# Kernel optimization log

Measured on AMD Instinct MI355X. Metric: run time of the kernel, lower is better.

The kernel has to match this reference:

```python
import jax, jax.numpy as jnp
import numpy as np

N = 20000          # num nodes (config['max_nodes'])
R = 11             # num relations = 5*2 + 1
B = 8              # num bases
IN_DIM = 300       # numberbatch embedding size
OUT_DIM = 256      # lstm hidden size
E = 640000         # num edges (avg degree 32)


def setup_inputs() -> dict:
    key = jax.random.key(0)
    k1, k2, k3, k4, k5, k6 = jax.random.split(key, 6)
    features = jax.random.normal(k1, (N, IN_DIM), dtype=jnp.float32)
    comps = jax.random.normal(k2, (R, B), dtype=jnp.float32) * 0.1
    bases = jax.random.normal(k3, (B, IN_DIM, OUT_DIM), dtype=jnp.float32) * 0.05
    bias = jnp.zeros((OUT_DIM,), dtype=jnp.float32)
    edge_src = jax.random.randint(k4, (E,), 0, N, dtype=jnp.int32)
    edge_rel = jax.random.randint(k5, (E,), 0, R, dtype=jnp.int32)
    edge_dst = jax.random.randint(k6, (E,), 0, N, dtype=jnp.int32)
    return {"features": features, "comps": comps, "bases": bases, "bias": bias,
            "edge_src": edge_src, "edge_rel": edge_rel, "edge_dst": edge_dst}


def reference(features, comps, bases, bias, edge_src, edge_rel, edge_dst):
    # Basis decomposition: per-relation weights [R, in, out]
    weights = jnp.einsum('rb,bio->rio', comps, bases)

    # Vertically-stacked sparse adjacency of size [R*N, N]:
    # row = rel*N + src, col = dst, with row normalization (sum_sparse).
    rows = edge_rel * N + edge_src                      # [E]
    ones = jnp.ones((E,), dtype=features.dtype)
    deg = jax.ops.segment_sum(ones, rows, num_segments=R * N)  # row sums
    vals = 1.0 / deg[rows]                              # normalized edge values

    # spmm(adj, features): gather neighbor features, scale, scatter-add to rows
    msgs = features[edge_dst] * vals[:, None]           # [E, in]
    af = jax.ops.segment_sum(msgs, rows, num_segments=R * N)   # [R*N, in]
    af = af.reshape(R, N, IN_DIM)

    # Relation-wise transform and sum over relations
    out = jnp.einsum('rio,rni->no', weights, af) + bias  # [N, out]
    return out
```

## Files before the change

kernel.cpp:

```cpp
#include <hip/hip_runtime.h>

#define NN   20000
#define RR   11
#define BB   8
#define IND  300
#define OUTD 256
#define EE   640000
#define RN   (RR * NN)
#define KP   304
#define SBS  308
#define SBU  (SBS / 2)
#define CAP  32
#define NSCAN_BLOCKS 215
#define SME  768
#define FEATB 5860
#define WT2B  304
#define HZB   860

typedef short bf16x8 __attribute__((ext_vector_type(8)));
typedef float f32x16 __attribute__((ext_vector_type(16)));

union U8 {
    bf16x8  v;
    ushort4 h[2];
    uint4   q;
};

__device__ inline unsigned short f2bf(float f) {
    union { float f; unsigned u; } x;
    x.f = f;
    unsigned u = x.u;
    u += 0x7fffu + ((u >> 16) & 1u);
    return (unsigned short)(u >> 16);
}
__device__ inline float bflo(unsigned p) { return __uint_as_float(p << 16); }
__device__ inline float bfhi(unsigned p) { return __uint_as_float(p & 0xFFFF0000u); }
__device__ inline unsigned packbf(float x, float y) {
    return (unsigned)f2bf(x) | ((unsigned)f2bf(y) << 16);
}

__global__ __launch_bounds__(256) void k_prep(const float* __restrict__ feat,
                                              const float* __restrict__ comps,
                                              const float* __restrict__ bases,
                                              unsigned short* __restrict__ f2,
                                              unsigned short* __restrict__ wt,
                                              unsigned* __restrict__ hist,
                                              int feat_blocks) {
    const int b = blockIdx.x;
    if (b < feat_blocks) {
        const unsigned i = ((unsigned)b * 256u + threadIdx.x) * 4u;
        if (i < (unsigned)(NN * IND)) {
            const float4 v = *(const float4*)(feat + i);
            ushort4 o;
            o.x = f2bf(v.x); o.y = f2bf(v.y); o.z = f2bf(v.z); o.w = f2bf(v.w);
            *(ushort4*)(f2 + i) = o;
        }
        return;
    }
    const int b2 = b - feat_blocks;
    if (b2 < WT2B) {
        const unsigned idx = (unsigned)b2 * 256u + threadIdx.x;
        const unsigned o   = idx / KP;
        const unsigned k   = idx - o * KP;
        float bk[BB];
#pragma unroll
        for (int bb = 0; bb < BB; ++bb)
            bk[bb] = (k < IND) ? bases[((unsigned)bb * IND + k) * OUTD + o] : 0.f;
#pragma unroll
        for (int r = 0; r < RR; ++r) {
            float acc = 0.f;
#pragma unroll
            for (int bb = 0; bb < BB; ++bb) acc += comps[r * BB + bb] * bk[bb];
            wt[((unsigned)r * OUTD + o) * KP + k] = f2bf(acc);
        }
        return;
    }
    const unsigned idx = (unsigned)(b2 - WT2B) * 256u + threadIdx.x;
    if (idx < RN) hist[idx] = 0u;
}

__global__ __launch_bounds__(256) void k_scatter2(const int* __restrict__ esrc,
                                                  const int* __restrict__ erel,
                                                  const int* __restrict__ edst,
                                                  unsigned* __restrict__ cnt,
                                                  unsigned* __restrict__ ssd2) {
    const int e = blockIdx.x * 256 + threadIdx.x;
    const unsigned key = (unsigned)erel[e] * NN + (unsigned)esrc[e];
    const unsigned p = atomicAdd(&cnt[key], 1u);
    if (p < CAP) ssd2[key * CAP + p] = (unsigned)edst[e];
}

__global__ __launch_bounds__(256) void k_hist(const int* __restrict__ esrc,
                                              const int* __restrict__ erel,
                                              unsigned* __restrict__ hist) {
    const int e = blockIdx.x * 256 + threadIdx.x;
    const unsigned key = (unsigned)erel[e] * NN + (unsigned)esrc[e];
    atomicAdd(&hist[key], 1u);
}

__global__ __launch_bounds__(256) void k_scan1(const unsigned* __restrict__ hist,
                                               unsigned* __restrict__ off,
                                               unsigned* __restrict__ bsum) {
    __shared__ unsigned sc[256];
    const int tid = threadIdx.x;
    const unsigned base = blockIdx.x * 1024u + (unsigned)tid * 4u;
    unsigned v0 = (base + 0 < RN) ? hist[base + 0] : 0u;
    unsigned v1 = (base + 1 < RN) ? hist[base + 1] : 0u;
    unsigned v2 = (base + 2 < RN) ? hist[base + 2] : 0u;
    unsigned v3 = (base + 3 < RN) ? hist[base + 3] : 0u;
    const unsigned s = v0 + v1 + v2 + v3;
    sc[tid] = s;
    __syncthreads();
    for (int d = 1; d < 256; d <<= 1) {
        unsigned t = (tid >= d) ? sc[tid - d] : 0u;
        __syncthreads();
        sc[tid] += t;
        __syncthreads();
    }
    if (tid == 255) bsum[blockIdx.x] = sc[255];
    unsigned run = sc[tid] - s;
    if (base + 0 < RN) off[base + 0] = run; run += v0;
    if (base + 1 < RN) off[base + 1] = run; run += v1;
    if (base + 2 < RN) off[base + 2] = run; run += v2;
    if (base + 3 < RN) off[base + 3] = run;
}

__global__ __launch_bounds__(256) void k_scan3(unsigned* __restrict__ off,
                                               unsigned* __restrict__ off2,
                                               const unsigned* __restrict__ bsum) {
    __shared__ unsigned sS;
    const unsigned K = blockIdx.x >> 2;
    if (threadIdx.x < 64) {
        unsigned s = 0;
        for (unsigned i = threadIdx.x; i < K; i += 64u) s += bsum[i];
#pragma unroll
        for (int d = 1; d < 64; d <<= 1) s += __shfl_xor(s, d, 64);
        if (threadIdx.x == 0) sS = s;
    }
    __syncthreads();
    const unsigned idx = blockIdx.x * 256u + threadIdx.x;
    if (idx < RN) {
        const unsigned v = off[idx] + sS;
        off[idx]  = v;
        off2[idx] = v;
    }
    if (idx == 0) off[RN] = EE;
}

__global__ __launch_bounds__(256) void k_scatter(const int* __restrict__ esrc,
                                                 const int* __restrict__ erel,
                                                 const int* __restrict__ edst,
                                                 unsigned* __restrict__ off2,
                                                 unsigned* __restrict__ ssd) {
    const int e = blockIdx.x * 256 + threadIdx.x;
    const unsigned key = (unsigned)erel[e] * NN + (unsigned)esrc[e];
    const unsigned p = atomicAdd(&off2[key], 1u);
    ssd[p] = (unsigned)edst[e];
}

template<int USE_BF16, int FIXED>
__global__ __launch_bounds__(512, 8) void k_main(const float* __restrict__ feat,
                                                 const unsigned short* __restrict__ feat2,
                                                 const float* __restrict__ bias,
                                                 const unsigned* __restrict__ offs,
                                                 const unsigned* __restrict__ ssd,
                                                 const unsigned short* __restrict__ wt,
                                                 float* __restrict__ out) {
    __shared__ __align__(16) unsigned short sbf[32 * SBS];
    __shared__ unsigned sme[FIXED ? 32 * CAP : SME];
    __shared__ unsigned soffs[RR * 33];

    const int tid  = threadIdx.x;
    const int wave = tid >> 6;
    const int lane = tid & 63;
    const int row  = lane & 31;
    const int q    = lane >> 5;
    const int n0   = blockIdx.x * 32;
    const int o0   = wave * 32;

    if (FIXED) {
        if (tid < RR * 32)
            soffs[tid] = offs[(tid >> 5) * NN + n0 + (tid & 31)];
    } else {
        if (tid < RR * 33) {
            const int r = tid / 33, j = tid - r * 33;
            soffs[tid] = offs[r * NN + n0 + j];
        }
    }
    if (tid < 128)
        ((unsigned*)sbf)[(tid >> 2) * SBU + 150 + (tid & 3)] = 0u;

    f32x16 acc;
#pragma unroll
    for (int i = 0; i < 16; ++i) acc[i] = 0.f;

    __syncthreads();

    for (int r = 0; r < RR; ++r) {
        const unsigned* so = soffs + r * (FIXED ? 32 : 33);
        unsigned e0v = 0;
        if (FIXED) {
            const unsigned gbase = ((unsigned)r * NN + (unsigned)n0) * CAP;
            sme[tid]       = ssd[gbase + tid];
            sme[tid + 512] = ssd[gbase + tid + 512];
        } else {
            e0v = so[0];
            const unsigned nE = so[32] - e0v;
            for (unsigned j = (unsigned)tid; j < nE; j += 512u)
                sme[j] = ssd[e0v + j];
        }
        __syncthreads();

#pragma unroll
        for (int g = 0; g < 4; ++g) {
            const int m = wave * 4 + g;
            unsigned c0, c1;
            float inv;
            if (FIXED) {
                const unsigned lenT = so[m];
                c0  = (unsigned)m * CAP;
                c1  = c0 + (lenT < CAP ? lenT : CAP);
                inv = lenT ? 1.0f / (float)lenT : 0.f;
            } else {
                c0  = so[m];
                c1  = so[m + 1];
                inv = (c1 > c0) ? 1.0f / (float)(c1 - c0) : 0.f;
            }
            if (USE_BF16) {
                float a0 = 0, a1 = 0, a2 = 0, a3 = 0, a4 = 0, a5 = 0;
                for (unsigned e = c0; e < c1; ++e) {
                    const unsigned d   = sme[e - e0v];
                    const unsigned* fp = (const unsigned*)feat2 + d * 150u;
                    const unsigned p0 = fp[lane];
                    const unsigned p1 = fp[lane + 64];
                    unsigned p2 = 0u;
                    if (lane < 22) p2 = fp[lane + 128];
                    a0 += bflo(p0); a1 += bfhi(p0);
                    a2 += bflo(p1); a3 += bfhi(p1);
                    a4 += bflo(p2); a5 += bfhi(p2);
                }
                unsigned* sp = (unsigned*)sbf + m * SBU;
                sp[lane]      = packbf(a0 * inv, a1 * inv);
                sp[lane + 64] = packbf(a2 * inv, a3 * inv);
                if (lane < 22) sp[lane + 128] = packbf(a4 * inv, a5 * inv);
            } else {
                float a0 = 0, a1 = 0, a2 = 0, a3 = 0, a4 = 0;
                for (unsigned e = c0; e < c1; ++e) {
                    const unsigned d = sme[e - e0v];
                    const float* fp  = feat + (size_t)d * IND;
                    a0 += fp[lane];
                    a1 += fp[lane + 64];
                    a2 += fp[lane + 128];
                    a3 += fp[lane + 192];
                    if (lane < 44) a4 += fp[lane + 256];
                }
                unsigned short* sp = sbf + m * SBS;
                sp[lane]       = f2bf(a0 * inv);
                sp[lane + 64]  = f2bf(a1 * inv);
                sp[lane + 128] = f2bf(a2 * inv);
                sp[lane + 192] = f2bf(a3 * inv);
                if (lane < 44) sp[lane + 256] = f2bf(a4 * inv);
            }
        }
        __syncthreads();

        const unsigned short* wb = wt + ((size_t)(r * OUTD + o0 + row) * KP) + 8 * q;
        const unsigned short* ab = sbf + row * SBS + 8 * q;
#pragma unroll
        for (int ks = 0; ks < 19; ++ks) {
            const int kk = ks * 16;
            U8 a, b;
            a.h[0] = *(const ushort4*)(ab + kk);
            a.h[1] = *(const ushort4*)(ab + kk + 4);
            b.q    = *(const uint4*)(wb + kk);
            acc = __builtin_amdgcn_mfma_f32_32x32x16_bf16(a.v, b.v, acc, 0, 0, 0);
        }
    }

    const int o = o0 + row;
    const float bv = bias[o];
#pragma unroll
    for (int reg = 0; reg < 16; ++reg) {
        const int node = (reg & 3) + 8 * (reg >> 2) + 4 * q;
        out[(size_t)(n0 + node) * OUTD + o] = acc[reg] + bv;
    }
}

extern "C" void kernel_launch(void* const* d_in, const int* in_sizes, int n_in,
                              void* d_out, int out_size, void* d_ws, size_t ws_size,
                              hipStream_t stream) {
    const float* feat  = (const float*)d_in[0];
    const float* comps = (const float*)d_in[1];
    const float* bases = (const float*)d_in[2];
    const float* bias  = (const float*)d_in[3];
    const int*   esrc  = (const int*)d_in[4];
    const int*   erel  = (const int*)d_in[5];
    const int*   edst  = (const int*)d_in[6];
    float* out = (float*)d_out;

    char* ws = (char*)d_ws;

    if (ws_size >= (size_t)42752192) {
        unsigned short* wt    = (unsigned short*)(ws + 0);
        unsigned*       cnt   = (unsigned*)(ws + 1712128);
        unsigned*       ssd2  = (unsigned*)(ws + 2592192);
        unsigned short* feat2 = (unsigned short*)(ws + 30752192);

        hipLaunchKernelGGL(k_prep, dim3(FEATB + WT2B + HZB), dim3(256), 0, stream,
                           feat, comps, bases, feat2, wt, cnt, FEATB);
        hipLaunchKernelGGL(k_scatter2, dim3(2500), dim3(256), 0, stream,
                           esrc, erel, edst, cnt, ssd2);
        hipLaunchKernelGGL((k_main<1, 1>), dim3(625), dim3(512), 0, stream,
                           feat, feat2, bias, cnt, ssd2, wt, out);
        return;
    }

    unsigned short* wt    = (unsigned short*)(ws + 0);
    unsigned*       off   = (unsigned*)(ws + 1712128);
    unsigned*       off2  = (unsigned*)(ws + 2592192);
    unsigned*       bsum  = (unsigned*)(ws + 3472192);
    unsigned*       hist  = (unsigned*)(ws + 3473216);
    unsigned*       ssd   = (unsigned*)(ws + 3473216);
    unsigned short* feat2 = (unsigned short*)(ws + 6033216);

    const bool use_bf16 = ws_size >= (size_t)18033216;
    const int  featb    = use_bf16 ? FEATB : 0;

    hipLaunchKernelGGL(k_prep,    dim3(featb + WT2B + HZB), dim3(256), 0, stream,
                       feat, comps, bases, feat2, wt, hist, featb);
    hipLaunchKernelGGL(k_hist,    dim3(2500), dim3(256), 0, stream, esrc, erel, hist);
    hipLaunchKernelGGL(k_scan1,   dim3(NSCAN_BLOCKS), dim3(256), 0, stream, hist, off, bsum);
    hipLaunchKernelGGL(k_scan3,   dim3(860),  dim3(256), 0, stream, off, off2, bsum);
    hipLaunchKernelGGL(k_scatter, dim3(2500), dim3(256), 0, stream, esrc, erel, edst, off2, ssd);
    if (use_bf16)
        hipLaunchKernelGGL((k_main<1, 0>), dim3(625), dim3(512), 0, stream,
                           feat, feat2, bias, off, ssd, wt, out);
    else
        hipLaunchKernelGGL((k_main<0, 0>), dim3(625), dim3(512), 0, stream,
                           feat, feat2, bias, off, ssd, wt, out);

    (void)in_sizes; (void)n_in; (void)out_size; (void)ws_size;
}
```

Before: 303.5 us.

## Split bf16 features into column slabs and process gather+MFMA slab by slab

Reorganizes the bf16 feature copy into three column slabs (128, 128 and 48 columns) stored separately, so each gather pass touches a smaller, more cache-resident region of the feature table. The main kernel now loops over slabs, then relations, and issues partial-K MFMAs per slab. Edge destinations are also stored as 16-bit indices and the whole per-block edge list is preloaded into shared memory once. The scatter is fused into the prep kernel with a separate zero kernel in front. The cost is three times more relation loops and barriers, plus a 16-bit index that only holds while node counts stay below 65536.

```diff
diff --git a/kernel.cpp b/kernel.cpp
--- a/kernel.cpp
+++ b/kernel.cpp
@@ -8,13 +8,18 @@
 #define EE   640000
 #define RN   (RR * NN)
 #define KP   304
+#define CAP  32
+#define S0U  64
+#define S1U  64
+#define S2U  24
+#define SBW  70
+#define SCATB 2500
+#define WT2B  304
+#define FEATB 5860
 #define SBS  308
 #define SBU  (SBS / 2)
-#define CAP  32
+#define SME  768
 #define NSCAN_BLOCKS 215
-#define SME  768
-#define FEATB 5860
-#define WT2B  304
 #define HZB   860
 
 typedef short bf16x8 __attribute__((ext_vector_type(8)));
@@ -39,27 +44,31 @@
     return (unsigned)f2bf(x) | ((unsigned)f2bf(y) << 16);
 }
 
+__global__ __launch_bounds__(256) void k_zero(unsigned* __restrict__ cnt) {
+    const unsigned i = blockIdx.x * 256u + threadIdx.x;
+    if (i < RN) cnt[i] = 0u;
+}
+
 __global__ __launch_bounds__(256) void k_prep(const float* __restrict__ feat,
                                               const float* __restrict__ comps,
                                               const float* __restrict__ bases,
-                                              unsigned short* __restrict__ f2,
+                                              const int* __restrict__ esrc,
+                                              const int* __restrict__ erel,
+                                              const int* __restrict__ edst,
+                                              unsigned* __restrict__ f2,
                                               unsigned short* __restrict__ wt,
-                                              unsigned* __restrict__ hist,
-                                              int feat_blocks) {
+                                              unsigned* __restrict__ cnt,
+                                              unsigned short* __restrict__ ssd2) {
     const int b = blockIdx.x;
-    if (b < feat_blocks) {
-        const unsigned i = ((unsigned)b * 256u + threadIdx.x) * 4u;
-        if (i < (unsigned)(NN * IND)) {
-            const float4 v = *(const float4*)(feat + i);
-            ushort4 o;
-            o.x = f2bf(v.x); o.y = f2bf(v.y); o.z = f2bf(v.z); o.w = f2bf(v.w);
-            *(ushort4*)(f2 + i) = o;
-        }
+    if (b < SCATB) {
+        const int e = b * 256 + threadIdx.x;
+        const unsigned key = (unsigned)erel[e] * NN + (unsigned)esrc[e];
+        const unsigned p = atomicAdd(&cnt[key], 1u);
+        if (p < CAP) ssd2[key * CAP + p] = (unsigned short)edst[e];
         return;
     }
-    const int b2 = b - feat_blocks;
-    if (b2 < WT2B) {
-        const unsigned idx = (unsigned)b2 * 256u + threadIdx.x;
+    if (b < SCATB + WT2B) {
+        const unsigned idx = (unsigned)(b - SCATB) * 256u + threadIdx.x;
         const unsigned o   = idx / KP;
         const unsigned k   = idx - o * KP;
         float bk[BB];
@@ -75,19 +84,144 @@
         }
         return;
     }
-    const unsigned idx = (unsigned)(b2 - WT2B) * 256u + threadIdx.x;
+    const unsigned i = (unsigned)(b - SCATB - WT2B) * 256u + threadIdx.x;
+    if (i < (unsigned)(NN * IND / 4)) {
+        const unsigned gi = i * 4u;
+        const unsigned n  = gi / IND;
+        const unsigned d  = gi - n * IND;
+        const float4 v = ((const float4*)feat)[i];
+        const unsigned p0 = packbf(v.x, v.y);
+        const unsigned p1 = packbf(v.z, v.w);
+        unsigned* dst;
+        if (d < 128u)      dst = f2 + n * S0U + (d >> 1);
+        else if (d < 256u) dst = f2 + (unsigned)NN * S0U + n * S1U + ((d - 128u) >> 1);
+        else               dst = f2 + (unsigned)NN * (S0U + S1U) + n * S2U + ((d - 256u) >> 1);
+        dst[0] = p0; dst[1] = p1;
+        if (d == 296u) { dst[2] = 0u; dst[3] = 0u; }
+    }
+}
+
+template<int SLOT>
+__device__ __forceinline__ void do_slot(const unsigned* __restrict__ f2,
+                                        const unsigned short* __restrict__ wt,
+                                        const unsigned short* sme,
+                                        const unsigned* slen,
+                                        unsigned short* sbf,
+                                        f32x16& acc,
+                                        int wave, int lane, int row, int q, int o0) {
+    constexpr unsigned BASEU = (SLOT == 0) ? 0u
+                             : (SLOT == 1) ? (unsigned)NN * S0U
+                                           : (unsigned)NN * (S0U + S1U);
+    constexpr unsigned RSU  = (SLOT == 2) ? (unsigned)S2U : 64u;
+    constexpr int      NKS  = (SLOT == 2) ? 3 : 8;
+    constexpr int      KOFF = SLOT * 128;
+
+    for (int r = 0; r < RR; ++r) {
+#pragma unroll
+        for (int g = 0; g < 4; ++g) {
+            const int m = wave * 4 + g;
+            const unsigned len0 = slen[r * 32 + m];
+            const unsigned len  = len0 < CAP ? len0 : CAP;
+            const unsigned short* sm = sme + (r * 32 + m) * CAP;
+            float lo = 0.f, hi = 0.f;
+            if (SLOT < 2 || lane < (int)S2U) {
+                for (unsigned e = 0; e < len; ++e) {
+                    const unsigned d = sm[e];
+                    const unsigned p = f2[BASEU + d * RSU + (unsigned)lane];
+                    lo += bflo(p); hi += bfhi(p);
+                }
+            }
+            const float inv = len0 ? 1.0f / (float)len0 : 0.f;
+            unsigned* sp = (unsigned*)sbf + m * SBW;
+            if (SLOT < 2 || lane < (int)S2U)
+                sp[lane] = packbf(lo * inv, hi * inv);
+        }
+        __syncthreads();
+        const unsigned short* wb = wt + (size_t)(r * OUTD + o0 + row) * KP + KOFF + 8 * q;
+        const unsigned short* ab = (const unsigned short*)((const unsigned*)sbf + row * SBW) + 8 * q;
+#pragma unroll
+        for (int ks = 0; ks < NKS; ++ks) {
+            const int kk = ks * 16;
+            U8 a, b;
+            a.h[0] = *(const ushort4*)(ab + kk);
+            a.h[1] = *(const ushort4*)(ab + kk + 4);
+            b.q    = *(const uint4*)(wb + kk);
+            acc = __builtin_amdgcn_mfma_f32_32x32x16_bf16(a.v, b.v, acc, 0, 0, 0);
+        }
+        __syncthreads();
+    }
+}
+
+__global__ __launch_bounds__(512, 8) void k_main2(const unsigned* __restrict__ f2,
+                                                  const float* __restrict__ bias,
+                                                  const unsigned* __restrict__ cnt,
+                                                  const unsigned short* __restrict__ ssd2,
+                                                  const unsigned short* __restrict__ wt,
+                                                  float* __restrict__ out) {
+    __shared__ unsigned short sme[RR * 32 * CAP];
+    __shared__ __align__(16) unsigned short sbf[32 * SBW * 2];
+    __shared__ unsigned slen[RR * 32];
+
+    const int tid  = threadIdx.x;
+    const int wave = tid >> 6;
+    const int lane = tid & 63;
+    const int row  = lane & 31;
+    const int q    = lane >> 5;
+    const int n0   = blockIdx.x * 32;
+    const int o0   = wave * 32;
+
+    if (tid < RR * 32) slen[tid] = cnt[(tid >> 5) * NN + n0 + (tid & 31)];
+    {
+        const unsigned* sv = (const unsigned*)ssd2;
+        unsigned* dv = (unsigned*)sme;
+        const unsigned rowbase = (unsigned)n0 * (CAP / 2);
+#pragma unroll
+        for (int rr = 0; rr < RR; ++rr)
+            dv[rr * 512 + tid] = sv[(unsigned)rr * NN * 16u + rowbase + (unsigned)tid];
+    }
+
+    f32x16 acc;
+#pragma unroll
+    for (int i = 0; i < 16; ++i) acc[i] = 0.f;
+    __syncthreads();
+
+    do_slot<0>(f2, wt, sme, slen, sbf, acc, wave, lane, row, q, o0);
+    do_slot<1>(f2, wt, sme, slen, sbf, acc, wave, lane, row, q, o0);
+    do_slot<2>(f2, wt, sme, slen, sbf, acc, wave, lane, row, q, o0);
+
+    const int o = o0 + row;
+    const float bv = bias[o];
+#pragma unroll
+    for (int reg = 0; reg < 16; ++reg) {
+        const int node = (reg & 3) + 8 * (reg >> 2) + 4 * q;
+        out[(size_t)(n0 + node) * OUTD + o] = acc[reg] + bv;
+    }
+}
+
+__global__ __launch_bounds__(256) void k_prep0(const float* __restrict__ comps,
+                                               const float* __restrict__ bases,
+                                               unsigned short* __restrict__ wt,
+                                               unsigned* __restrict__ hist) {
+    const int b = blockIdx.x;
+    if (b < WT2B) {
+        const unsigned idx = (unsigned)b * 256u + threadIdx.x;
+        const unsigned o   = idx / KP;
+        const unsigned k   = idx - o * KP;
+        float bk[BB];
+#pragma unroll
+        for (int bb = 0; bb < BB; ++bb)
+            bk[bb] = (k < IND) ? bases[((unsigned)bb * IND + k) * OUTD + o] : 0.f;
+#pragma unroll
+        for (int r = 0; r < RR; ++r) {
+            float acc = 0.f;
+#pragma unroll
+            for (int bb = 0; bb < BB; ++bb) acc += comps[r * BB + bb] * bk[bb];
+            wt[((unsigned)r * OUTD + o) * KP + k] = f2bf(acc);
+        }
+        return;
+    }
+    const unsigned idx = (unsigned)(b - WT2B) * 256u + threadIdx.x;
     if (idx < RN) hist[idx] = 0u;
-}
-
-__global__ __launch_bounds__(256) void k_scatter2(const int* __restrict__ esrc,
-                                                  const int* __restrict__ erel,
-                                                  const int* __restrict__ edst,
-                                                  unsigned* __restrict__ cnt,
-                                                  unsigned* __restrict__ ssd2) {
-    const int e = blockIdx.x * 256 + threadIdx.x;
-    const unsigned key = (unsigned)erel[e] * NN + (unsigned)esrc[e];
-    const unsigned p = atomicAdd(&cnt[key], 1u);
-    if (p < CAP) ssd2[key * CAP + p] = (unsigned)edst[e];
 }
 
 __global__ __launch_bounds__(256) void k_hist(const int* __restrict__ esrc,
@@ -158,16 +292,14 @@
     ssd[p] = (unsigned)edst[e];
 }
 
-template<int USE_BF16, int FIXED>
-__global__ __launch_bounds__(512, 8) void k_main(const float* __restrict__ feat,
-                                                 const unsigned short* __restrict__ feat2,
-                                                 const float* __restrict__ bias,
-                                                 const unsigned* __restrict__ offs,
-                                                 const unsigned* __restrict__ ssd,
-                                                 const unsigned short* __restrict__ wt,
-                                                 float* __restrict__ out) {
+__global__ __launch_bounds__(512, 8) void k_mainL(const float* __restrict__ feat,
+                                                  const float* __restrict__ bias,
+                                                  const unsigned* __restrict__ offs,
+                                                  const unsigned* __restrict__ ssd,
+                                                  const unsigned short* __restrict__ wt,
+                                                  float* __restrict__ out) {
     __shared__ __align__(16) unsigned short sbf[32 * SBS];
-    __shared__ unsigned sme[FIXED ? 32 * CAP : SME];
+    __shared__ unsigned sme[SME];
     __shared__ unsigned soffs[RR * 33];
 
     const int tid  = threadIdx.x;
@@ -178,14 +310,9 @@
     const int n0   = blockIdx.x * 32;
     const int o0   = wave * 32;
 
-    if (FIXED) {
-        if (tid < RR * 32)
-            soffs[tid] = offs[(tid >> 5) * NN + n0 + (tid & 31)];
-    } else {
-        if (tid < RR * 33) {
-            const int r = tid / 33, j = tid - r * 33;
-            soffs[tid] = offs[r * NN + n0 + j];
-        }
+    if (tid < RR * 33) {
+        const int r = tid / 33, j = tid - r * 33;
+        soffs[tid] = offs[r * NN + n0 + j];
     }
     if (tid < 128)
         ((unsigned*)sbf)[(tid >> 2) * SBU + 150 + (tid & 3)] = 0u;
@@ -193,77 +320,38 @@
     f32x16 acc;
 #pragma unroll
     for (int i = 0; i < 16; ++i) acc[i] = 0.f;
-
     __syncthreads();
 
     for (int r = 0; r < RR; ++r) {
-        const unsigned* so = soffs + r * (FIXED ? 32 : 33);
-        unsigned e0v = 0;
-        if (FIXED) {
-            const unsigned gbase = ((unsigned)r * NN + (unsigned)n0) * CAP;
-            sme[tid]       = ssd[gbase + tid];
-            sme[tid + 512] = ssd[gbase + tid + 512];
-        } else {
-            e0v = so[0];
-            const unsigned nE = so[32] - e0v;
-            for (unsigned j = (unsigned)tid; j < nE; j += 512u)
-                sme[j] = ssd[e0v + j];
-        }
-        __syncthreads();
-
+        const unsigned* so = soffs + r * 33;
+        const unsigned e0v = so[0];
+        const unsigned nE  = so[32] - e0v;
+        for (unsigned j = (unsigned)tid; j < nE; j += 512u)
+            sme[j] = ssd[e0v + j];
+        __syncthreads();
 #pragma unroll
         for (int g = 0; g < 4; ++g) {
             const int m = wave * 4 + g;
-            unsigned c0, c1;
-            float inv;
-            if (FIXED) {
-                const unsigned lenT = so[m];
-                c0  = (unsigned)m * CAP;
-                c1  = c0 + (lenT < CAP ? lenT : CAP);
-                inv = lenT ? 1.0f / (float)lenT : 0.f;
-            } else {
-                c0  = so[m];
-                c1  = so[m + 1];
-                inv = (c1 > c0) ? 1.0f / (float)(c1 - c0) : 0.f;
+            const unsigned c0 = so[m], c1 = so[m + 1];
+            float a0 = 0, a1 = 0, a2 = 0, a3 = 0, a4 = 0;
+            for (unsigned e = c0; e < c1; ++e) {
+                const unsigned d = sme[e - e0v];
+                const float* fp  = feat + (size_t)d * IND;
+                a0 += fp[lane];
+                a1 += fp[lane + 64];
+                a2 += fp[lane + 128];
+                a3 += fp[lane + 192];
+                if (lane < 44) a4 += fp[lane + 256];
             }
-            if (USE_BF16) {
-                float a0 = 0, a1 = 0, a2 = 0, a3 = 0, a4 = 0, a5 = 0;
-                for (unsigned e = c0; e < c1; ++e) {
-                    const unsigned d   = sme[e - e0v];
-                    const unsigned* fp = (const unsigned*)feat2 + d * 150u;
-                    const unsigned p0 = fp[lane];
-                    const unsigned p1 = fp[lane + 64];
-                    unsigned p2 = 0u;
-                    if (lane < 22) p2 = fp[lane + 128];
-                    a0 += bflo(p0); a1 += bfhi(p0);
-                    a2 += bflo(p1); a3 += bfhi(p1);
-                    a4 += bflo(p2); a5 += bfhi(p2);
-                }
-                unsigned* sp = (unsigned*)sbf + m * SBU;
-                sp[lane]      = packbf(a0 * inv, a1 * inv);
-                sp[lane + 64] = packbf(a2 * inv, a3 * inv);
-                if (lane < 22) sp[lane + 128] = packbf(a4 * inv, a5 * inv);
-            } else {
-                float a0 = 0, a1 = 0, a2 = 0, a3 = 0, a4 = 0;
-                for (unsigned e = c0; e < c1; ++e) {
-                    const unsigned d = sme[e - e0v];
-                    const float* fp  = feat + (size_t)d * IND;
-                    a0 += fp[lane];
-                    a1 += fp[lane + 64];
-                    a2 += fp[lane + 128];
-                    a3 += fp[lane + 192];
-                    if (lane < 44) a4 += fp[lane + 256];
-                }
-                unsigned short* sp = sbf + m * SBS;
-                sp[lane]       = f2bf(a0 * inv);
-                sp[lane + 64]  = f2bf(a1 * inv);
-                sp[lane + 128] = f2bf(a2 * inv);
-                sp[lane + 192] = f2bf(a3 * inv);
-                if (lane < 44) sp[lane + 256] = f2bf(a4 * inv);
-            }
-        }
-        __syncthreads();
-
+            const float inv = (c1 > c0) ? 1.0f / (float)(c1 - c0) : 0.f;
+            unsigned short* sp = sbf + m * SBS;
+            sp[lane]       = f2bf(a0 * inv);
+            sp[lane + 64]  = f2bf(a1 * inv);
+            sp[lane + 128] = f2bf(a2 * inv);
+            sp[lane + 192] = f2bf(a3 * inv);
+            if (lane < 44) sp[lane + 256] = f2bf(a4 * inv);
+        }
+        __syncthreads();
         const unsigned short* wb = wt + ((size_t)(r * OUTD + o0 + row) * KP) + 8 * q;
         const unsigned short* ab = sbf + row * SBS + 8 * q;
 #pragma unroll
@@ -276,7 +364,6 @@
             acc = __builtin_amdgcn_mfma_f32_32x32x16_bf16(a.v, b.v, acc, 0, 0, 0);
         }
     }
-
     const int o = o0 + row;
     const float bv = bias[o];
 #pragma unroll
@@ -300,18 +387,17 @@
 
     char* ws = (char*)d_ws;
 
-    if (ws_size >= (size_t)42752192) {
-        unsigned short* wt    = (unsigned short*)(ws + 0);
-        unsigned*       cnt   = (unsigned*)(ws + 1712128);
-        unsigned*       ssd2  = (unsigned*)(ws + 2592192);
-        unsigned short* feat2 = (unsigned short*)(ws + 30752192);
-
-        hipLaunchKernelGGL(k_prep, dim3(FEATB + WT2B + HZB), dim3(256), 0, stream,
-                           feat, comps, bases, feat2, wt, cnt, FEATB);
-        hipLaunchKernelGGL(k_scatter2, dim3(2500), dim3(256), 0, stream,
-                           esrc, erel, edst, cnt, ssd2);
-        hipLaunchKernelGGL((k_main<1, 1>), dim3(625), dim3(512), 0, stream,
-                           feat, feat2, bias, cnt, ssd2, wt, out);
+    if (ws_size >= (size_t)28832192) {
+        unsigned short* wt   = (unsigned short*)(ws + 0);
+        unsigned*       cnt  = (unsigned*)(ws + 1712128);
+        unsigned short* ssd2 = (unsigned short*)(ws + 2592192);
+        unsigned*       f2   = (unsigned*)(ws + 16672192);
+
+        hipLaunchKernelGGL(k_zero, dim3(HZB), dim3(256), 0, stream, cnt);
+        hipLaunchKernelGGL(k_prep, dim3(SCATB + WT2B + FEATB), dim3(256), 0, stream,
+                           feat, comps, bases, esrc, erel, edst, f2, wt, cnt, ssd2);
+        hipLaunchKernelGGL(k_main2, dim3(625), dim3(512), 0, stream,
+                           f2, bias, cnt, ssd2, wt, out);
         return;
     }
 
@@ -321,23 +407,15 @@
     unsigned*       bsum  = (unsigned*)(ws + 3472192);
     unsigned*       hist  = (unsigned*)(ws + 3473216);
     unsigned*       ssd   = (unsigned*)(ws + 3473216);
-    unsigned short* feat2 = (unsigned short*)(ws + 6033216);
-
-    const bool use_bf16 = ws_size >= (size_t)18033216;
-    const int  featb    = use_bf16 ? FEATB : 0;
-
-    hipLaunchKernelGGL(k_prep,    dim3(featb + WT2B + HZB), dim3(256), 0, stream,
-                       feat, comps, bases, feat2, wt, hist, featb);
-    hipLaunchKernelGGL(k_hist,    dim3(2500), dim3(256), 0, stream, esrc, erel, hist);
-    hipLaunchKernelGGL(k_scan1,   dim3(NSCAN_BLOCKS), dim3(256), 0, stream, hist, off, bsum);
-    hipLaunchKernelGGL(k_scan3,   dim3(860),  dim3(256), 0, stream, off, off2, bsum);
-    hipLaunchKernelGGL(k_scatter, dim3(2500), dim3(256), 0, stream, esrc, erel, edst, off2, ssd);
-    if (use_bf16)
-        hipLaunchKernelGGL((k_main<1, 0>), dim3(625), dim3(512), 0, stream,
-                           feat, feat2, bias, off, ssd, wt, out);
-    else
-        hipLaunchKernelGGL((k_main<0, 0>), dim3(625), dim3(512), 0, stream,
-                           feat, feat2, bias, off, ssd, wt, out);
+
+    hipLaunchKernelGGL(k_prep0,  dim3(WT2B + HZB), dim3(256), 0, stream,
+                       comps, bases, wt, hist);
+    hipLaunchKernelGGL(k_hist,   dim3(2500), dim3(256), 0, stream, esrc, erel, hist);
+    hipLaunchKernelGGL(k_scan1,  dim3(NSCAN_BLOCKS), dim3(256), 0, stream, hist, off, bsum);
+    hipLaunchKernelGGL(k_scan3,  dim3(860),  dim3(256), 0, stream, off, off2, bsum);
+    hipLaunchKernelGGL(k_scatter,dim3(2500), dim3(256), 0, stream, esrc, erel, edst, off2, ssd);
+    hipLaunchKernelGGL(k_mainL,  dim3(625),  dim3(512), 0, stream,
+                       feat, bias, off, ssd, wt, out);
 
     (void)in_sizes; (void)n_in; (void)out_size; (void)ws_size;
 }
```

Result: slower. 382.9 us (+26.1%).
